# Kernel optimization log

Measured on AMD Instinct MI355X. Metric: run time of the kernel, lower is better.

Reference implementation:

```python
import jax, jax.numpy as jnp
import numpy as np

BITS = 4
PACK = 32 // BITS          # 8 values per int32
MAXQ = (1 << BITS) - 1     # 0xF
GROUP_SIZE = 128


def _unpack_rows(packed):
    # packed: [K//PACK, N] int32 -> [K, N] int32 (nibbles along K)
    shifts = (jnp.arange(PACK, dtype=jnp.int32) * BITS)  # [PACK]
    vals = (packed[:, None, :] >> shifts[None, :, None]) & MAXQ
    return vals.reshape(packed.shape[0] * PACK, packed.shape[1])


def _unpack_cols(packed):
    # packed: [G, N//PACK] int32 -> [G, N] int32 (nibbles along N)
    shifts = (jnp.arange(PACK, dtype=jnp.int32) * BITS)  # [PACK]
    vals = (packed[:, :, None] >> shifts[None, None, :]) & MAXQ
    return vals.reshape(packed.shape[0], packed.shape[1] * PACK)


def setup_inputs() -> dict:
    key = jax.random.key(0)
    k1, k2, k3, k4 = jax.random.split(key, 4)
    B, S, K, N = 4, 2048, 4096, 11008
    G = K // GROUP_SIZE  # 32
    x = jax.random.normal(k1, (B, S, K), dtype=jnp.float32)
    qweight = jax.random.randint(k2, (K // PACK, N), 0, 2**31 - 1, dtype=jnp.int32)
    qzeros = jax.random.randint(k3, (G, N // PACK), 0, 2**31 - 1, dtype=jnp.int32)
    scales = jax.random.uniform(k4, (G, N), dtype=jnp.float32) * 0.01 + 0.001
    return {"x": x, "qweight": qweight, "qzeros": qzeros, "scales": scales}


def reference(x, qweight, qzeros, scales):
    K = qweight.shape[0] * PACK
    q = _unpack_rows(qweight)                 # [K, N] int in [0, 15]
    z = _unpack_cols(qzeros) + 1              # [G, N], GPTQ stores zero-1
    g_idx = jnp.arange(K, dtype=jnp.int32) // GROUP_SIZE  # [K]
    # fused dequant: W[k, n] = scale[g(k), n] * (q[k, n] - zero[g(k), n])
    W = (q - z[g_idx]).astype(x.dtype) * scales[g_idx]    # [K, N]
    return jnp.einsum('bsk,kn->bsn', x, W)
```

## Files before the change

kernel.cpp:

```cpp
#include <hip/hip_runtime.h>


typedef __bf16 bf16;
typedef __attribute__((ext_vector_type(8))) __bf16 bf16x8;
typedef __attribute__((ext_vector_type(4))) __bf16 bf16x4;
typedef __attribute__((ext_vector_type(4))) float floatx4;

constexpr int KDIM = 4096;
constexpr int NDIM = 11008;
constexpr int GROUP = 128;
constexpr int BM = 128, BN = 128, BK = 64;
constexpr int NBX = NDIM / BN;

__global__ __launch_bounds__(256)
void cvt_x(const float* __restrict__ x, bf16* __restrict__ xb) {
  const int idx = (blockIdx.x * 256 + threadIdx.x) * 8;
  const float4 a = *(const float4*)&x[idx];
  const float4 b = *(const float4*)&x[idx + 4];
  bf16x8 pk = { (bf16)a.x, (bf16)a.y, (bf16)a.z, (bf16)a.w,
                (bf16)b.x, (bf16)b.y, (bf16)b.z, (bf16)b.w };
  *(bf16x8*)&xb[idx] = pk;
}

__global__ __launch_bounds__(256)
void dequant_wt(const int* __restrict__ qweight, const int* __restrict__ qzeros,
                const float* __restrict__ scales, bf16* __restrict__ wt) {
  const int n = blockIdx.x * 256 + threadIdx.x;
  const int g = blockIdx.y;
  const float sc = scales[g * NDIM + n];
  const unsigned zw = (unsigned)qzeros[g * (NDIM / 8) + (n >> 3)];
  const float zs = (float)(((zw >> ((n & 7) * 4)) & 0xF) + 1) * sc;
  const int kp0 = (g * GROUP) >> 3;
  const int obase = n * KDIM + g * GROUP;
#pragma unroll
  for (int i = 0; i < 16; ++i) {
    const unsigned w = (unsigned)qweight[(kp0 + i) * NDIM + n];
    bf16x8 pk;
#pragma unroll
    for (int j = 0; j < 8; ++j)
      pk[j] = (bf16)((float)((w >> (4 * j)) & 0xF) * sc - zs);
    *(bf16x8*)&wt[obase + i * 8] = pk;
  }
}

__global__ __launch_bounds__(256)
void gemm_bf16(const bf16* __restrict__ A, const bf16* __restrict__ BT,
               float* __restrict__ out) {
  __shared__ bf16 As[BM * BK];
  __shared__ bf16 Bs[BN * BK];

  const int tid  = threadIdx.x;
  const int lane = tid & 63;
  const int wave = tid >> 6;
  const int quad = lane >> 4;
  const int l16  = lane & 15;
  const int wm   = (wave >> 1) * 64;
  const int wn   = (wave & 1) * 64;

  const int nwg = gridDim.x * gridDim.y;
  const int orig = blockIdx.y * gridDim.x + blockIdx.x;
  int wg = orig;
  if ((nwg & 7) == 0) wg = (orig & 7) * (nwg >> 3) + (orig >> 3);
  const int bx = wg % NBX;
  const int by = wg / NBX;
  const int row0 = by * BM;
  const int col0 = bx * BN;

  const int srow   = lane >> 3;
  const int schunk = (lane & 7) ^ srow;
  const int soff   = srow * KDIM + schunk * 8;

  floatx4 acc[4][4];
#pragma unroll
  for (int i = 0; i < 4; ++i)
#pragma unroll
    for (int j = 0; j < 4; ++j) acc[i][j] = (floatx4)0.f;

  for (int ks = 0; ks < KDIM / BK; ++ks) {
    const int k0 = ks * BK;
#pragma unroll
    for (int t4 = 0; t4 < 4; ++t4) {
      const int t = wave * 4 + t4;
      const int ga = (row0 + t * 8) * KDIM + k0 + soff;
      __builtin_amdgcn_global_load_lds(
          (const __attribute__((address_space(1))) void*)(A + ga),
          (__attribute__((address_space(3))) void*)&As[t * 8 * BK], 16, 0, 0);
      const int gb = (col0 + t * 8) * KDIM + k0 + soff;
      __builtin_amdgcn_global_load_lds(
          (const __attribute__((address_space(1))) void*)(BT + gb),
          (__attribute__((address_space(3))) void*)&Bs[t * 8 * BK], 16, 0, 0);
    }
    __syncthreads();

#pragma unroll
    for (int kk = 0; kk < 2; ++kk) {
      bf16x8 af[4], bfr[4];
#pragma unroll
      for (int i = 0; i < 4; ++i) {
        const int r = wm + i * 16 + l16;
        af[i] = *(bf16x8*)&As[r * BK + (((kk * 4 + quad) ^ (r & 7)) << 3)];
      }
#pragma unroll
      for (int j = 0; j < 4; ++j) {
        const int r = wn + j * 16 + l16;
        bfr[j] = *(bf16x8*)&Bs[r * BK + (((kk * 4 + quad) ^ (r & 7)) << 3)];
      }
#pragma unroll
      for (int i = 0; i < 4; ++i)
#pragma unroll
        for (int j = 0; j < 4; ++j)
          acc[i][j] = __builtin_amdgcn_mfma_f32_16x16x32_bf16(af[i], bfr[j], acc[i][j], 0, 0, 0);
    }
    __syncthreads();
  }

#pragma unroll
  for (int i = 0; i < 4; ++i) {
#pragma unroll
    for (int j = 0; j < 4; ++j) {
      const int r0 = row0 + wm + i * 16 + quad * 4;
      const int c  = col0 + wn + j * 16 + l16;
#pragma unroll
      for (int r = 0; r < 4; ++r)
        out[(r0 + r) * NDIM + c] = acc[i][j][r];
    }
  }
}

__global__ __launch_bounds__(256)
void gptq_gemm(const float* __restrict__ x, const int* __restrict__ qweight,
               const int* __restrict__ qzeros, const float* __restrict__ scales,
               float* __restrict__ out) {
  constexpr int FBK = 32;
  constexpr int LDT = 40;
  __shared__ bf16 As[BM * LDT];
  __shared__ bf16 Bs[BN * LDT];

  const int tid  = threadIdx.x;
  const int lane = tid & 63;
  const int wave = tid >> 6;
  const int quad = lane >> 4;
  const int l16  = lane & 15;
  const int wm   = (wave >> 1) * 64;
  const int wn   = (wave & 1) * 64;

  const int row0 = blockIdx.y * BM;
  const int col0 = blockIdx.x * BN;

  const int nb   = tid & 127;
  const int kpl0 = tid >> 7;
  const int gn   = col0 + nb;

  floatx4 acc[4][4];
#pragma unroll
  for (int i = 0; i < 4; ++i)
#pragma unroll
    for (int j = 0; j < 4; ++j) acc[i][j] = (floatx4)0.f;

  const int NGROUPS = KDIM / GROUP;

  for (int g = 0; g < NGROUPS; ++g) {
    const float sc = scales[g * NDIM + gn];
    const unsigned int zw = (unsigned int)qzeros[g * (NDIM / 8) + (gn >> 3)];
    const int z = (int)((zw >> ((gn & 7) * 4)) & 0xF) + 1;
    const float zs = (float)z * sc;

    for (int kk = 0; kk < GROUP / FBK; ++kk) {
      const int k0 = g * GROUP + kk * FBK;
#pragma unroll
      for (int r = 0; r < 4; ++r) {
        const int flat = r * 256 + tid;
        const int m  = flat >> 3;
        const int k4 = (flat & 7) << 2;
        const float4 v = *(const float4*)&x[(row0 + m) * KDIM + k0 + k4];
        bf16x4 pk = { (bf16)v.x, (bf16)v.y, (bf16)v.z, (bf16)v.w };
        *(bf16x4*)&As[m * LDT + k4] = pk;
      }
      const int kp0 = k0 >> 3;
#pragma unroll
      for (int w = 0; w < 2; ++w) {
        const int kpl = kpl0 + w * 2;
        const unsigned int word = (unsigned int)qweight[(kp0 + kpl) * NDIM + gn];
        bf16x8 pk;
#pragma unroll
        for (int j = 0; j < 8; ++j) {
          const float q = (float)((word >> (4 * j)) & 0xF);
          pk[j] = (bf16)(q * sc - zs);
        }
        const int sw = kpl ^ ((nb >> 3) & 3);
        *(bf16x8*)&Bs[nb * LDT + sw * 8] = pk;
      }
      __syncthreads();
      bf16x8 af[4], bfr[4];
#pragma unroll
      for (int i = 0; i < 4; ++i)
        af[i] = *(bf16x8*)&As[(wm + i * 16 + l16) * LDT + quad * 8];
#pragma unroll
      for (int j = 0; j < 4; ++j) {
        const int nr = wn + j * 16 + l16;
        const int sw = quad ^ ((nr >> 3) & 3);
        bfr[j] = *(bf16x8*)&Bs[nr * LDT + sw * 8];
      }
#pragma unroll
      for (int i = 0; i < 4; ++i)
#pragma unroll
        for (int j = 0; j < 4; ++j)
          acc[i][j] = __builtin_amdgcn_mfma_f32_16x16x32_bf16(af[i], bfr[j], acc[i][j], 0, 0, 0);
      __syncthreads();
    }
  }
#pragma unroll
  for (int i = 0; i < 4; ++i) {
#pragma unroll
    for (int j = 0; j < 4; ++j) {
      const int r0 = row0 + wm + i * 16 + quad * 4;
      const int c  = col0 + wn + j * 16 + l16;
#pragma unroll
      for (int r = 0; r < 4; ++r)
        out[(r0 + r) * NDIM + c] = acc[i][j][r];
    }
  }
}

extern "C" void kernel_launch(void* const* d_in, const int* in_sizes, int n_in,
                              void* d_out, int out_size, void* d_ws, size_t ws_size,
                              hipStream_t stream) {
  const float* x       = (const float*)d_in[0];
  const int*   qweight = (const int*)d_in[1];
  const int*   qzeros  = (const int*)d_in[2];
  const float* scales  = (const float*)d_in[3];
  float*       out     = (float*)d_out;

  const int M = in_sizes[0] / KDIM;

  const size_t xb_bytes = (size_t)M * KDIM * sizeof(bf16);
  const size_t wt_bytes = (size_t)NDIM * KDIM * sizeof(bf16);

  if (d_ws && ws_size >= xb_bytes + wt_bytes && (M % BM) == 0 &&
      ((M * KDIM) % (8 * 256)) == 0) {
    bf16* xb = (bf16*)d_ws;
    bf16* wt = (bf16*)((char*)d_ws + xb_bytes);
    cvt_x<<<(M * KDIM) / (8 * 256), 256, 0, stream>>>(x, xb);
    dequant_wt<<<dim3(NDIM / 256, KDIM / GROUP), 256, 0, stream>>>(qweight, qzeros, scales, wt);
    gemm_bf16<<<dim3(NDIM / BN, M / BM), 256, 0, stream>>>(xb, wt, out);
  } else {
    gptq_gemm<<<dim3(NDIM / BN, M / BM), 256, 0, stream>>>(x, qweight, qzeros, scales, out);
  }
}
```

Measured before the change: 1.324 ms.

## Rewrite bf16 GEMM as 256x256 tile, 8-wave, 4-stage pipelined kernel

The bf16 GEMM moves from 128x128 tiles with 4 waves and a single LDS buffer to 256x256 tiles with 8 waves, BK=32 and a 4-slot LDS ring. Async global-to-LDS loads are issued three steps ahead and guarded by explicit vmcnt waits, with split barriers and s_setprio around the MFMA bursts. The dequant kernel is also remapped so each wave writes one contiguous transposed weight row. The aim is to hide memory latency and raise data reuse per tile, at the cost of more LDS and registers per block and a stricter M%256 requirement.

```diff
diff --git a/kernel.cpp b/kernel.cpp
--- a/kernel.cpp
+++ b/kernel.cpp
@@ -9,8 +9,8 @@
 constexpr int KDIM = 4096;
 constexpr int NDIM = 11008;
 constexpr int GROUP = 128;
-constexpr int BM = 128, BN = 128, BK = 64;
-constexpr int NBX = NDIM / BN;
+constexpr int NT = KDIM / 32;
+constexpr int NBX = NDIM / 256;
 
 __global__ __launch_bounds__(256)
 void cvt_x(const float* __restrict__ x, bf16* __restrict__ xb) {
@@ -25,29 +25,148 @@
 __global__ __launch_bounds__(256)
 void dequant_wt(const int* __restrict__ qweight, const int* __restrict__ qzeros,
                 const float* __restrict__ scales, bf16* __restrict__ wt) {
-  const int n = blockIdx.x * 256 + threadIdx.x;
-  const int g = blockIdx.y;
-  const float sc = scales[g * NDIM + n];
-  const unsigned zw = (unsigned)qzeros[g * (NDIM / 8) + (n >> 3)];
-  const float zs = (float)(((zw >> ((n & 7) * 4)) & 0xF) + 1) * sc;
-  const int kp0 = (g * GROUP) >> 3;
-  const int obase = n * KDIM + g * GROUP;
-#pragma unroll
-  for (int i = 0; i < 16; ++i) {
-    const unsigned w = (unsigned)qweight[(kp0 + i) * NDIM + n];
+  const int n    = (blockIdx.x << 2) | (threadIdx.x >> 6);
+  const int lane = threadIdx.x & 63;
+#pragma unroll
+  for (int it = 0; it < 8; ++it) {
+    const int kw = it * 64 + lane;
+    const int g  = kw >> 4;
+    const float sc = scales[g * NDIM + n];
+    const unsigned zw = (unsigned)qzeros[g * (NDIM / 8) + (n >> 3)];
+    const float zs = (float)(((zw >> ((n & 7) * 4)) & 0xF) + 1) * sc;
+    const unsigned w = (unsigned)qweight[kw * NDIM + n];
     bf16x8 pk;
 #pragma unroll
     for (int j = 0; j < 8; ++j)
       pk[j] = (bf16)((float)((w >> (4 * j)) & 0xF) * sc - zs);
-    *(bf16x8*)&wt[obase + i * 8] = pk;
-  }
-}
-
-__global__ __launch_bounds__(256)
+    *(bf16x8*)&wt[(long)n * KDIM + kw * 8] = pk;
+  }
+}
+
+
+#define GWINDOW(T, DO_STAGE, VM)                                               \
+  {                                                                            \
+    const int slot_ = (T) & 3;                                                 \
+    const bf16* __restrict__ Asl = &As[slot_][0];                              \
+    const bf16* __restrict__ Bsl = &Bs[slot_][0];                              \
+           \
+    _Pragma("unroll") for (int i = 0; i < 4; ++i)                              \
+      af[i] = *(const bf16x8*)&Asl[(arow0 + i * 16) * 32 + csw];               \
+    _Pragma("unroll") for (int j = 0; j < 4; ++j)                              \
+      bfr[j] = *(const bf16x8*)&Bsl[(brow0 + j * 16) * 32 + csw];              \
+    if (DO_STAGE) { STAGE_A((T) + 3, 0); STAGE_A((T) + 3, 1); }                \
+    __builtin_amdgcn_s_barrier();                                              \
+    __builtin_amdgcn_s_setprio(1);                                             \
+    _Pragma("unroll") for (int i = 0; i < 4; ++i)                              \
+      _Pragma("unroll") for (int j = 0; j < 4; ++j)                            \
+        acc[i][j] = __builtin_amdgcn_mfma_f32_16x16x32_bf16(af[i], bfr[j],     \
+                                                            acc[i][j], 0, 0, 0);\
+    __builtin_amdgcn_s_setprio(0);                                             \
+    __builtin_amdgcn_s_barrier();                                              \
+               \
+    _Pragma("unroll") for (int i = 0; i < 4; ++i)                              \
+      af[i] = *(const bf16x8*)&Asl[(arow0 + 64 + i * 16) * 32 + csw];          \
+    if (DO_STAGE) { STAGE_B((T) + 3, 0); STAGE_B((T) + 3, 1); }                \
+    __builtin_amdgcn_s_barrier();                                              \
+    __builtin_amdgcn_s_setprio(1);                                             \
+    _Pragma("unroll") for (int i = 0; i < 4; ++i)                              \
+      _Pragma("unroll") for (int j = 0; j < 4; ++j)                            \
+        acc[4 + i][j] = __builtin_amdgcn_mfma_f32_16x16x32_bf16(af[i], bfr[j], \
+                                                          acc[4 + i][j], 0, 0, 0);\
+    __builtin_amdgcn_s_setprio(0);                                             \
+    if ((VM) == 8)      asm volatile("s_waitcnt vmcnt(8)" ::: "memory");       \
+    else if ((VM) == 4) asm volatile("s_waitcnt vmcnt(4)" ::: "memory");       \
+    else if ((VM) == 0) asm volatile("s_waitcnt vmcnt(0)" ::: "memory");       \
+    __builtin_amdgcn_s_barrier();                                              \
+  }
+
+#define STAGE_A(T, HALF)                                                       \
+  __builtin_amdgcn_global_load_lds(                                            \
+      (const __attribute__((address_space(1))) void*)(Ag + (long)(T) * 32 +    \
+                                                      (long)(HALF) * 128 * KDIM),\
+      (__attribute__((address_space(3))) void*)&As[(T) & 3][(HALF) * 4096 +    \
+                                                            wave * 512],       \
+      16, 0, 0)
+#define STAGE_B(T, HALF)                                                       \
+  __builtin_amdgcn_global_load_lds(                                            \
+      (const __attribute__((address_space(1))) void*)(Bg + (long)(T) * 32 +    \
+                                                      (long)(HALF) * 128 * KDIM),\
+      (__attribute__((address_space(3))) void*)&Bs[(T) & 3][(HALF) * 4096 +    \
+                                                            wave * 512],       \
+      16, 0, 0)
+
+__global__ __launch_bounds__(512, 2)
 void gemm_bf16(const bf16* __restrict__ A, const bf16* __restrict__ BT,
                float* __restrict__ out) {
-  __shared__ bf16 As[BM * BK];
-  __shared__ bf16 Bs[BN * BK];
+  __shared__ bf16 As[4][256 * 32];
+  __shared__ bf16 Bs[4][256 * 32];
+
+  const int tid  = threadIdx.x;
+  const int lane = tid & 63;
+  const int wave = tid >> 6;
+  const int quad = lane >> 4;
+  const int l16  = lane & 15;
+  const int wr   = wave >> 2;
+  const int wc   = wave & 3;
+
+  const int nwg  = gridDim.x * gridDim.y;
+  const int orig = blockIdx.y * gridDim.x + blockIdx.x;
+  const int wg   = ((nwg & 7) == 0) ? (orig & 7) * (nwg >> 3) + (orig >> 3) : orig;
+  const int bx   = wg % NBX;
+  const int by   = wg / NBX;
+  const int row0 = by * 256;
+  const int col0 = bx * 256;
+
+  const int srow = lane >> 2;
+  const int sch  = (lane & 3) ^ ((lane >> 3) & 3);
+  const bf16* Ag = A  + (long)(row0 + wave * 16 + srow) * KDIM + sch * 8;
+  const bf16* Bg = BT + (long)(col0 + wave * 16 + srow) * KDIM + sch * 8;
+
+  const int csw   = (quad ^ ((l16 >> 1) & 3)) << 3;
+  const int arow0 = wr * 128 + l16;
+  const int brow0 = wc * 64 + l16;
+
+  floatx4 acc[8][4];
+#pragma unroll
+  for (int i = 0; i < 8; ++i)
+#pragma unroll
+    for (int j = 0; j < 4; ++j) acc[i][j] = (floatx4)0.f;
+
+  bf16x8 af[4], bfr[4];
+
+#pragma unroll
+  for (int t = 0; t < 3; ++t) {
+    STAGE_A(t, 0); STAGE_A(t, 1); STAGE_B(t, 0); STAGE_B(t, 1);
+  }
+  asm volatile("s_waitcnt vmcnt(8)" ::: "memory");
+  __builtin_amdgcn_s_barrier();
+
+  int t = 0;
+  for (; t < NT - 3; ++t) GWINDOW(t, true, 8);
+  GWINDOW(t, false, 4); ++t;
+  GWINDOW(t, false, 0); ++t;
+  GWINDOW(t, false, -1);
+
+#pragma unroll
+  for (int mf = 0; mf < 8; ++mf) {
+#pragma unroll
+    for (int j = 0; j < 4; ++j) {
+      const int r0 = row0 + wr * 128 + mf * 16 + quad * 4;
+      const int c  = col0 + wc * 64 + j * 16 + l16;
+#pragma unroll
+      for (int r = 0; r < 4; ++r)
+        out[(long)(r0 + r) * NDIM + c] = acc[mf][j][r];
+    }
+  }
+}
+
+__global__ __launch_bounds__(256)
+void gptq_gemm(const float* __restrict__ x, const int* __restrict__ qweight,
+               const int* __restrict__ qzeros, const float* __restrict__ scales,
+               float* __restrict__ out) {
+  constexpr int BM = 128, BN = 128, FBK = 32, LDT = 40;
+  __shared__ bf16 Asf[BM * LDT];
+  __shared__ bf16 Bsf[BN * LDT];
 
   const int tid  = threadIdx.x;
   const int lane = tid & 63;
@@ -57,93 +176,6 @@
   const int wm   = (wave >> 1) * 64;
   const int wn   = (wave & 1) * 64;
 
-  const int nwg = gridDim.x * gridDim.y;
-  const int orig = blockIdx.y * gridDim.x + blockIdx.x;
-  int wg = orig;
-  if ((nwg & 7) == 0) wg = (orig & 7) * (nwg >> 3) + (orig >> 3);
-  const int bx = wg % NBX;
-  const int by = wg / NBX;
-  const int row0 = by * BM;
-  const int col0 = bx * BN;
-
-  const int srow   = lane >> 3;
-  const int schunk = (lane & 7) ^ srow;
-  const int soff   = srow * KDIM + schunk * 8;
-
-  floatx4 acc[4][4];
-#pragma unroll
-  for (int i = 0; i < 4; ++i)
-#pragma unroll
-    for (int j = 0; j < 4; ++j) acc[i][j] = (floatx4)0.f;
-
-  for (int ks = 0; ks < KDIM / BK; ++ks) {
-    const int k0 = ks * BK;
-#pragma unroll
-    for (int t4 = 0; t4 < 4; ++t4) {
-      const int t = wave * 4 + t4;
-      const int ga = (row0 + t * 8) * KDIM + k0 + soff;
-      __builtin_amdgcn_global_load_lds(
-          (const __attribute__((address_space(1))) void*)(A + ga),
-          (__attribute__((address_space(3))) void*)&As[t * 8 * BK], 16, 0, 0);
-      const int gb = (col0 + t * 8) * KDIM + k0 + soff;
-      __builtin_amdgcn_global_load_lds(
-          (const __attribute__((address_space(1))) void*)(BT + gb),
-          (__attribute__((address_space(3))) void*)&Bs[t * 8 * BK], 16, 0, 0);
-    }
-    __syncthreads();
-
-#pragma unroll
-    for (int kk = 0; kk < 2; ++kk) {
-      bf16x8 af[4], bfr[4];
-#pragma unroll
-      for (int i = 0; i < 4; ++i) {
-        const int r = wm + i * 16 + l16;
-        af[i] = *(bf16x8*)&As[r * BK + (((kk * 4 + quad) ^ (r & 7)) << 3)];
-      }
-#pragma unroll
-      for (int j = 0; j < 4; ++j) {
-        const int r = wn + j * 16 + l16;
-        bfr[j] = *(bf16x8*)&Bs[r * BK + (((kk * 4 + quad) ^ (r & 7)) << 3)];
-      }
-#pragma unroll
-      for (int i = 0; i < 4; ++i)
-#pragma unroll
-        for (int j = 0; j < 4; ++j)
-          acc[i][j] = __builtin_amdgcn_mfma_f32_16x16x32_bf16(af[i], bfr[j], acc[i][j], 0, 0, 0);
-    }
-    __syncthreads();
-  }
-
-#pragma unroll
-  for (int i = 0; i < 4; ++i) {
-#pragma unroll
-    for (int j = 0; j < 4; ++j) {
-      const int r0 = row0 + wm + i * 16 + quad * 4;
-      const int c  = col0 + wn + j * 16 + l16;
-#pragma unroll
-      for (int r = 0; r < 4; ++r)
-        out[(r0 + r) * NDIM + c] = acc[i][j][r];
-    }
-  }
-}
-
-__global__ __launch_bounds__(256)
-void gptq_gemm(const float* __restrict__ x, const int* __restrict__ qweight,
-               const int* __restrict__ qzeros, const float* __restrict__ scales,
-               float* __restrict__ out) {
-  constexpr int FBK = 32;
-  constexpr int LDT = 40;
-  __shared__ bf16 As[BM * LDT];
-  __shared__ bf16 Bs[BN * LDT];
-
-  const int tid  = threadIdx.x;
-  const int lane = tid & 63;
-  const int wave = tid >> 6;
-  const int quad = lane >> 4;
-  const int l16  = lane & 15;
-  const int wm   = (wave >> 1) * 64;
-  const int wn   = (wave & 1) * 64;
-
   const int row0 = blockIdx.y * BM;
   const int col0 = blockIdx.x * BN;
 
@@ -157,13 +189,10 @@
 #pragma unroll
     for (int j = 0; j < 4; ++j) acc[i][j] = (floatx4)0.f;
 
-  const int NGROUPS = KDIM / GROUP;
-
-  for (int g = 0; g < NGROUPS; ++g) {
+  for (int g = 0; g < KDIM / GROUP; ++g) {
     const float sc = scales[g * NDIM + gn];
     const unsigned int zw = (unsigned int)qzeros[g * (NDIM / 8) + (gn >> 3)];
-    const int z = (int)((zw >> ((gn & 7) * 4)) & 0xF) + 1;
-    const float zs = (float)z * sc;
+    const float zs = (float)((int)((zw >> ((gn & 7) * 4)) & 0xF) + 1) * sc;
 
     for (int kk = 0; kk < GROUP / FBK; ++kk) {
       const int k0 = g * GROUP + kk * FBK;
@@ -174,7 +203,7 @@
         const int k4 = (flat & 7) << 2;
         const float4 v = *(const float4*)&x[(row0 + m) * KDIM + k0 + k4];
         bf16x4 pk = { (bf16)v.x, (bf16)v.y, (bf16)v.z, (bf16)v.w };
-        *(bf16x4*)&As[m * LDT + k4] = pk;
+        *(bf16x4*)&Asf[m * LDT + k4] = pk;
       }
       const int kp0 = k0 >> 3;
 #pragma unroll
@@ -188,18 +217,18 @@
           pk[j] = (bf16)(q * sc - zs);
         }
         const int sw = kpl ^ ((nb >> 3) & 3);
-        *(bf16x8*)&Bs[nb * LDT + sw * 8] = pk;
+        *(bf16x8*)&Bsf[nb * LDT + sw * 8] = pk;
       }
       __syncthreads();
       bf16x8 af[4], bfr[4];
 #pragma unroll
       for (int i = 0; i < 4; ++i)
-        af[i] = *(bf16x8*)&As[(wm + i * 16 + l16) * LDT + quad * 8];
+        af[i] = *(bf16x8*)&Asf[(wm + i * 16 + l16) * LDT + quad * 8];
 #pragma unroll
       for (int j = 0; j < 4; ++j) {
         const int nr = wn + j * 16 + l16;
         const int sw = quad ^ ((nr >> 3) & 3);
-        bfr[j] = *(bf16x8*)&Bs[nr * LDT + sw * 8];
+        bfr[j] = *(bf16x8*)&Bsf[nr * LDT + sw * 8];
       }
 #pragma unroll
       for (int i = 0; i < 4; ++i)
@@ -236,14 +265,14 @@
   const size_t xb_bytes = (size_t)M * KDIM * sizeof(bf16);
   const size_t wt_bytes = (size_t)NDIM * KDIM * sizeof(bf16);
 
-  if (d_ws && ws_size >= xb_bytes + wt_bytes && (M % BM) == 0 &&
+  if (d_ws && ws_size >= xb_bytes + wt_bytes && (M % 256) == 0 &&
       ((M * KDIM) % (8 * 256)) == 0) {
     bf16* xb = (bf16*)d_ws;
     bf16* wt = (bf16*)((char*)d_ws + xb_bytes);
     cvt_x<<<(M * KDIM) / (8 * 256), 256, 0, stream>>>(x, xb);
-    dequant_wt<<<dim3(NDIM / 256, KDIM / GROUP), 256, 0, stream>>>(qweight, qzeros, scales, wt);
-    gemm_bf16<<<dim3(NDIM / BN, M / BM), 256, 0, stream>>>(xb, wt, out);
+    dequant_wt<<<NDIM / 4, 256, 0, stream>>>(qweight, qzeros, scales, wt);
+    gemm_bf16<<<dim3(NDIM / 256, M / 256), 512, 0, stream>>>(xb, wt, out);
   } else {
-    gptq_gemm<<<dim3(NDIM / BN, M / BM), 256, 0, stream>>>(x, qweight, qzeros, scales, out);
-  }
-}
+    gptq_gemm<<<dim3(NDIM / 128, M / 128), 256, 0, stream>>>(x, qweight, qzeros, scales, out);
+  }
+}
```

Result: slower. 1.387 ms (+4.8%).
